# Performance work log

Measured on AMD Instinct MI355X. Metric: run time of the kernel, lower is better.

## Reference

```python
import jax, jax.numpy as jnp
import numpy as np

B, F, D_IN, H, OUT = 32768, 200, 5, 15, 30

def setup_inputs() -> dict:
    key = jax.random.key(0)
    ks = jax.random.split(key, 7)
    return {
        "y":  jax.random.normal(ks[0], (B, F, D_IN), dtype=jnp.float32),
        "W1": jax.random.normal(ks[1], (F, D_IN, H), dtype=jnp.float32) * 0.3,
        "b1": jax.random.normal(ks[2], (F, H), dtype=jnp.float32) * 0.1,
        "W2": jax.random.normal(ks[3], (F, H, OUT), dtype=jnp.float32) * 0.2,
        "b2": jax.random.normal(ks[4], (F, OUT), dtype=jnp.float32) * 0.1,
        "W3": jax.random.normal(ks[5], (F * OUT, 1), dtype=jnp.float32) * 0.02,
        "b3": jax.random.normal(ks[6], (1,), dtype=jnp.float32) * 0.1,
    }

def reference(y, W1, b1, W2, b2, W3, b3):
    # 200 independent tiny 2-layer MLPs, batched over the feature axis f.
    # Note: original applies ReLU only AFTER the second Linear.
    h1 = jnp.einsum('bfi,fih->bfh', y, W1) + b1          # [B, F, H]
    h2 = jax.nn.relu(jnp.einsum('bfh,fho->bfo', h1, W2) + b2)  # [B, F, OUT]
    flat = h2.reshape(h2.shape[0], -1)                   # concat along feature axis -> [B, F*OUT]
    return flat @ W3 + b3                                # [B, 1]
```

## Files before the change

kernel.cpp:

```cpp
#include <hip/hip_runtime.h>

#define B_TOTAL 32768
#define NF 200
#define D_IN 5
#define NH 15
#define NOUT 30

__global__ __launch_bounds__(256) void precompute_kernel(
    const float* __restrict__ W1, const float* __restrict__ b1,
    const float* __restrict__ W2, const float* __restrict__ b2,
    float* __restrict__ Wc, float* __restrict__ bc)
{
    int idx = blockIdx.x * 256 + threadIdx.x;
    if (idx < NF * D_IN * NOUT) {
        int o  = idx % NOUT;
        int fi = idx / NOUT;
        int i  = fi % D_IN;
        int f  = fi / D_IN;
        float s = 0.f;
        #pragma unroll
        for (int h = 0; h < NH; ++h)
            s = fmaf(W1[(f * D_IN + i) * NH + h], W2[(f * NH + h) * NOUT + o], s);
        Wc[idx] = s;
    } else if (idx < NF * D_IN * NOUT + NF * NOUT) {
        int k = idx - NF * D_IN * NOUT;
        int o = k % NOUT;
        int f = k / NOUT;
        float s = b2[f * NOUT + o];
        #pragma unroll
        for (int h = 0; h < NH; ++h)
            s = fmaf(b1[f * NH + h], W2[(f * NH + h) * NOUT + o], s);
        bc[k] = s;
    }
}

#define BTILE 64
#define NSUB 8
#define FC 40
#define NCHUNK 5
#define FSUB 5
#define ROWSTRIDE 201

__global__ __launch_bounds__(512, 4) void mlp_kernel(
    const float* __restrict__ y, const float* __restrict__ Wc,
    const float* __restrict__ bc, const float* __restrict__ w3,
    const float* __restrict__ b3, float* __restrict__ out)
{
    __shared__ float ytile[BTILE * ROWSTRIDE];
    __shared__ float red[BTILE * NSUB];

    const int tid     = threadIdx.x;
    const int b_local = tid & 63;
    const int sub     = tid >> 6;
    const int sub_u   = __builtin_amdgcn_readfirstlane(sub);
    const int b0      = blockIdx.x * BTILE;

    float acc = 0.f;

    for (int c = 0; c < NCHUNK; ++c) {
        for (int j = tid; j < BTILE * (FC * D_IN / 4); j += 512) {
            int row  = j / (FC * D_IN / 4);
            int col4 = j - row * (FC * D_IN / 4);
            const float4 v = *(const float4*)&y[(size_t)(b0 + row) * (NF * D_IN)
                                                + c * (FC * D_IN) + col4 * 4];
            float* dst = &ytile[row * ROWSTRIDE + col4 * 4];
            dst[0] = v.x; dst[1] = v.y; dst[2] = v.z; dst[3] = v.w;
        }
        __syncthreads();

        const float* yrow = &ytile[b_local * ROWSTRIDE + sub * (FSUB * D_IN)];
        const int fbase = c * FC + sub_u * FSUB;

        #pragma unroll 1
        for (int ff = 0; ff < FSUB; ++ff) {
            const int f = fbase + ff;
            const float y0 = yrow[ff * 5 + 0];
            const float y1 = yrow[ff * 5 + 1];
            const float y2 = yrow[ff * 5 + 2];
            const float y3 = yrow[ff * 5 + 3];
            const float y4 = yrow[ff * 5 + 4];
            const float* __restrict__ wf  = Wc + f * (D_IN * NOUT);
            const float* __restrict__ bcf = bc + f * NOUT;
            const float* __restrict__ w3f = w3 + f * NOUT;
            #pragma unroll
            for (int o = 0; o < NOUT; ++o) {
                float z = bcf[o];
                z = fmaf(y0, wf[o          ], z);
                z = fmaf(y1, wf[NOUT   + o ], z);
                z = fmaf(y2, wf[2*NOUT + o ], z);
                z = fmaf(y3, wf[3*NOUT + o ], z);
                z = fmaf(y4, wf[4*NOUT + o ], z);
                acc = fmaf(fmaxf(z, 0.f), w3f[o], acc);
            }
        }
        __syncthreads();
    }

    red[b_local * NSUB + sub] = acc;
    __syncthreads();
    if (tid < BTILE) {
        float s = b3[0];
        #pragma unroll
        for (int k = 0; k < NSUB; ++k) s += red[tid * NSUB + k];
        out[b0 + tid] = s;
    }
}

extern "C" void kernel_launch(void* const* d_in, const int* in_sizes, int n_in,
                              void* d_out, int out_size, void* d_ws, size_t ws_size,
                              hipStream_t stream) {
    const float* y  = (const float*)d_in[0];
    const float* W1 = (const float*)d_in[1];
    const float* b1 = (const float*)d_in[2];
    const float* W2 = (const float*)d_in[3];
    const float* b2 = (const float*)d_in[4];
    const float* W3 = (const float*)d_in[5];
    const float* b3 = (const float*)d_in[6];
    float* out = (float*)d_out;

    float* Wc = (float*)d_ws;
    float* bc = Wc + NF * D_IN * NOUT;

    const int total_pre = NF * D_IN * NOUT + NF * NOUT;
    precompute_kernel<<<(total_pre + 255) / 256, 256, 0, stream>>>(W1, b1, W2, b2, Wc, bc);
    mlp_kernel<<<B_TOTAL / BTILE, 512, 0, stream>>>(y, Wc, bc, W3, b3, out);
}
```

Measured before the change: 235.9 us.

## Stream y directly into registers and pack per-feature weights into records

New measurement: 298.5 us. +26.5%, slower.

```diff
diff --git a/kernel.cpp b/kernel.cpp
--- a/kernel.cpp
+++ b/kernel.cpp
@@ -5,99 +5,105 @@
 #define D_IN 5
 #define NH 15
 #define NOUT 30
+#define RECS 216
 
 __global__ __launch_bounds__(256) void precompute_kernel(
     const float* __restrict__ W1, const float* __restrict__ b1,
     const float* __restrict__ W2, const float* __restrict__ b2,
-    float* __restrict__ Wc, float* __restrict__ bc)
+    const float* __restrict__ W3, float* __restrict__ rec)
 {
-    int idx = blockIdx.x * 256 + threadIdx.x;
-    if (idx < NF * D_IN * NOUT) {
-        int o  = idx % NOUT;
-        int fi = idx / NOUT;
-        int i  = fi % D_IN;
-        int f  = fi / D_IN;
+    const int f = blockIdx.x;
+    const int t = threadIdx.x;
+    float* r = rec + f * RECS;
+    if (t < NOUT) {
+        const int o = t;
+        float s = b2[f * NOUT + o];
+        #pragma unroll
+        for (int h = 0; h < NH; ++h)
+            s = fmaf(b1[f * NH + h], W2[(f * NH + h) * NOUT + o], s);
+        r[o] = s;
+    } else if (t < 2 * NOUT) {
+        const int o = t - NOUT;
+        r[NOUT + o] = W3[f * NOUT + o];
+    } else if (t < 2 * NOUT + D_IN * NOUT) {
+        const int j = t - 2 * NOUT;
+        const int i = j / NOUT;
+        const int o = j - i * NOUT;
         float s = 0.f;
         #pragma unroll
         for (int h = 0; h < NH; ++h)
             s = fmaf(W1[(f * D_IN + i) * NH + h], W2[(f * NH + h) * NOUT + o], s);
-        Wc[idx] = s;
-    } else if (idx < NF * D_IN * NOUT + NF * NOUT) {
-        int k = idx - NF * D_IN * NOUT;
-        int o = k % NOUT;
-        int f = k / NOUT;
-        float s = b2[f * NOUT + o];
-        #pragma unroll
-        for (int h = 0; h < NH; ++h)
-            s = fmaf(b1[f * NH + h], W2[(f * NH + h) * NOUT + o], s);
-        bc[k] = s;
+        r[2 * NOUT + i * NOUT + o] = s;
     }
 }
 
 #define BTILE 64
-#define NSUB 8
-#define FC 40
+#define NSUB 10
+#define FSUB 20
 #define NCHUNK 5
-#define FSUB 5
-#define ROWSTRIDE 201
 
-__global__ __launch_bounds__(512, 4) void mlp_kernel(
-    const float* __restrict__ y, const float* __restrict__ Wc,
-    const float* __restrict__ bc, const float* __restrict__ w3,
+__global__ __launch_bounds__(640, 5) void mlp_kernel(
+    const float* __restrict__ y, const float* __restrict__ rec,
     const float* __restrict__ b3, float* __restrict__ out)
 {
-    __shared__ float ytile[BTILE * ROWSTRIDE];
     __shared__ float red[BTILE * NSUB];
 
-    const int tid     = threadIdx.x;
-    const int b_local = tid & 63;
-    const int sub     = tid >> 6;
-    const int sub_u   = __builtin_amdgcn_readfirstlane(sub);
-    const int b0      = blockIdx.x * BTILE;
+    const int tid  = threadIdx.x;
+    const int lane = tid & 63;
+    const int sub  = tid >> 6;
+    const int sub_u = __builtin_amdgcn_readfirstlane(sub);
+    const int b0   = blockIdx.x * BTILE;
+    const int b    = b0 + lane;
 
-    float acc = 0.f;
+    const float* yp   = y + (size_t)b * (NF * D_IN) + sub_u * (FSUB * D_IN);
+    const float* wrec = rec + sub_u * FSUB * RECS;
 
-    for (int c = 0; c < NCHUNK; ++c) {
-        for (int j = tid; j < BTILE * (FC * D_IN / 4); j += 512) {
-            int row  = j / (FC * D_IN / 4);
-            int col4 = j - row * (FC * D_IN / 4);
-            const float4 v = *(const float4*)&y[(size_t)(b0 + row) * (NF * D_IN)
-                                                + c * (FC * D_IN) + col4 * 4];
-            float* dst = &ytile[row * ROWSTRIDE + col4 * 4];
-            dst[0] = v.x; dst[1] = v.y; dst[2] = v.z; dst[3] = v.w;
+    const float4* yq = (const float4*)yp;
+    float4 c0 = yq[0], c1 = yq[1], c2 = yq[2], c3 = yq[3], c4 = yq[4];
+
+    float acc[4] = {0.f, 0.f, 0.f, 0.f};
+
+    #pragma unroll 1
+    for (int cc = 0; cc < NCHUNK; ++cc) {
+        float4 n0, n1, n2, n3, n4;
+        if (cc < NCHUNK - 1) {
+            const float4* nq = yq + (cc + 1) * 5;
+            n0 = nq[0]; n1 = nq[1]; n2 = nq[2]; n3 = nq[3]; n4 = nq[4];
+        } else {
+            n0 = c0; n1 = c1; n2 = c2; n3 = c3; n4 = c4;
         }
-        __syncthreads();
 
-        const float* yrow = &ytile[b_local * ROWSTRIDE + sub * (FSUB * D_IN)];
-        const int fbase = c * FC + sub_u * FSUB;
+        float yv[20];
+        *(float4*)&yv[0]  = c0;
+        *(float4*)&yv[4]  = c1;
+        *(float4*)&yv[8]  = c2;
+        *(float4*)&yv[12] = c3;
+        *(float4*)&yv[16] = c4;
 
-        #pragma unroll 1
-        for (int ff = 0; ff < FSUB; ++ff) {
-            const int f = fbase + ff;
-            const float y0 = yrow[ff * 5 + 0];
-            const float y1 = yrow[ff * 5 + 1];
-            const float y2 = yrow[ff * 5 + 2];
-            const float y3 = yrow[ff * 5 + 3];
-            const float y4 = yrow[ff * 5 + 4];
-            const float* __restrict__ wf  = Wc + f * (D_IN * NOUT);
-            const float* __restrict__ bcf = bc + f * NOUT;
-            const float* __restrict__ w3f = w3 + f * NOUT;
+        #pragma unroll
+        for (int k = 0; k < 4; ++k) {
+            const float* __restrict__ r = wrec + (cc * 4 + k) * RECS;
+            float z[NOUT];
             #pragma unroll
-            for (int o = 0; o < NOUT; ++o) {
-                float z = bcf[o];
-                z = fmaf(y0, wf[o          ], z);
-                z = fmaf(y1, wf[NOUT   + o ], z);
-                z = fmaf(y2, wf[2*NOUT + o ], z);
-                z = fmaf(y3, wf[3*NOUT + o ], z);
-                z = fmaf(y4, wf[4*NOUT + o ], z);
-                acc = fmaf(fmaxf(z, 0.f), w3f[o], acc);
+            for (int o = 0; o < NOUT; ++o) z[o] = r[o];
+            #pragma unroll
+            for (int i = 0; i < D_IN; ++i) {
+                const float yvi = yv[k * 5 + i];
+                #pragma unroll
+                for (int o = 0; o < NOUT; ++o)
+                    z[o] = fmaf(yvi, r[2 * NOUT + i * NOUT + o], z[o]);
             }
+            #pragma unroll
+            for (int o = 0; o < NOUT; ++o)
+                acc[o & 3] = fmaf(fmaxf(z[o], 0.f), r[NOUT + o], acc[o & 3]);
         }
-        __syncthreads();
+
+        c0 = n0; c1 = n1; c2 = n2; c3 = n3; c4 = n4;
     }
 
-    red[b_local * NSUB + sub] = acc;
+    red[lane * NSUB + sub] = (acc[0] + acc[1]) + (acc[2] + acc[3]);
     __syncthreads();
+
     if (tid < BTILE) {
         float s = b3[0];
         #pragma unroll
@@ -118,10 +124,8 @@
     const float* b3 = (const float*)d_in[6];
     float* out = (float*)d_out;
 
-    float* Wc = (float*)d_ws;
-    float* bc = Wc + NF * D_IN * NOUT;
+    float* rec = (float*)d_ws;
 
-    const int total_pre = NF * D_IN * NOUT + NF * NOUT;
-    precompute_kernel<<<(total_pre + 255) / 256, 256, 0, stream>>>(W1, b1, W2, b2, Wc, bc);
-    mlp_kernel<<<B_TOTAL / BTILE, 512, 0, stream>>>(y, Wc, bc, W3, b3, out);
+    precompute_kernel<<<NF, 256, 0, stream>>>(W1, b1, W2, b2, W3, rec);
+    mlp_kernel<<<B_TOTAL / BTILE, BTILE * NSUB, 0, stream>>>(y, rec, b3, out);
 }
```
